# Kernel tuning notes

Hardware: AMD Instinct MI355X
Metric: run time of the kernel (lower is better)

## Reference

```python
import jax, jax.numpy as jnp
import numpy as np

NUM_HEADS = 8
MODEL_DIM = 1024
SEQ_LEN = 2048


def setup_inputs() -> dict:
    key = jax.random.key(0)
    ks = jax.random.split(key, 9)
    H, D, L = NUM_HEADS, MODEL_DIM, SEQ_LEN
    s_in = 1.0 / np.sqrt(D)
    s_out = 1.0 / np.sqrt(H * D)
    return {
        "tokens": jax.random.normal(ks[0], (D, L), dtype=jnp.float32),
        "Wq": jax.random.uniform(ks[1], (H * D, D), jnp.float32, -s_in, s_in),
        "bq": jax.random.uniform(ks[2], (H * D,), jnp.float32, -s_in, s_in),
        "Wk": jax.random.uniform(ks[3], (H * D, D), jnp.float32, -s_in, s_in),
        "bk": jax.random.uniform(ks[4], (H * D,), jnp.float32, -s_in, s_in),
        "Wv": jax.random.uniform(ks[5], (H * D, D), jnp.float32, -s_in, s_in),
        "bv": jax.random.uniform(ks[6], (H * D,), jnp.float32, -s_in, s_in),
        "Wo": jax.random.uniform(ks[7], (D, H * D), jnp.float32, -s_out, s_out),
        "bo": jax.random.uniform(ks[8], (D,), jnp.float32, -s_out, s_out),
    }


def _split_heads(x, H, D, L):
    # Faithful to torch: raw .view of contiguous [H*D, L] into (L, H, D),
    # then permute(1, 2, 0) -> (H, D, L). This is a memory reinterpretation,
    # not a transpose, exactly as in the original module.
    return x.reshape(L, H, D).transpose(1, 2, 0)


def reference(tokens, Wq, bq, Wk, bk, Wv, bv, Wo, bo):
    D, L = tokens.shape
    H = Wq.shape[0] // D
    # 1x1 Conv1d == matmul over channel dim
    q = _split_heads(Wq @ tokens + bq[:, None], H, D, L)  # (H, D, L)
    k = _split_heads(Wk @ tokens + bk[:, None], H, D, L)  # (H, D, L)
    v = _split_heads(Wv @ tokens + bv[:, None], H, D, L)  # (H, D, L)
    scores = jnp.einsum("hdl,hdm->hlm", q, k) / np.sqrt(D)  # (H, L, L)
    # torch F.softmax without dim on a 3D tensor -> dim=0 (head axis)
    attn = jax.nn.softmax(scores, axis=0)
    ctx = jnp.einsum("hlm,hdm->hdl", attn, v)  # (H, D, L)
    out = Wo @ ctx.reshape(H * D, L) + bo[:, None]  # (D, L)
    return out
```

## Files before the change

### kernel.cpp

```cpp
#include <hip/hip_runtime.h>

#define SEQL 2048
#define DMODEL 1024
#define HDIM 8192

typedef unsigned short bf16_t;
typedef __attribute__((ext_vector_type(8))) short bf16x8;
typedef __attribute__((ext_vector_type(4))) float f32x4;

__device__ __forceinline__ bf16_t f2bf(float f) {
  unsigned u = __float_as_uint(f);
  u += 0x7fffu + ((u >> 16) & 1u);
  return (bf16_t)(u >> 16);
}
__device__ __forceinline__ float bf2f(bf16_t b) {
  return __uint_as_float(((unsigned)b) << 16);
}

__global__ __launch_bounds__(256) void cvt_f32_bf16(const float* __restrict__ in,
                                                    bf16_t* __restrict__ out, int n) {
  int i = (blockIdx.x * 256 + threadIdx.x) * 4;
  if (i >= n) return;
  float4 f = *reinterpret_cast<const float4*>(in + i);
  ushort4 u;
  u.x = f2bf(f.x); u.y = f2bf(f.y); u.z = f2bf(f.z); u.w = f2bf(f.w);
  *reinterpret_cast<ushort4*>(out + i) = u;
}

__global__ __launch_bounds__(256) void cvt3_f32_bf16(const float* __restrict__ a,
                                                     const float* __restrict__ b,
                                                     const float* __restrict__ c,
                                                     bf16_t* __restrict__ out) {
  const int SEG = HDIM * DMODEL;
  int i = (blockIdx.x * 256 + threadIdx.x) * 4;
  const float* src;
  int off;
  if (i < SEG) { src = a; off = i; }
  else if (i < 2 * SEG) { src = b; off = i - SEG; }
  else { src = c; off = i - 2 * SEG; }
  float4 f = *reinterpret_cast<const float4*>(src + off);
  ushort4 u;
  u.x = f2bf(f.x); u.y = f2bf(f.y); u.z = f2bf(f.z); u.w = f2bf(f.w);
  *reinterpret_cast<ushort4*>(out + i) = u;
}

__global__ __launch_bounds__(256) void bias3(const float* __restrict__ a,
                                             const float* __restrict__ b,
                                             const float* __restrict__ c,
                                             float* __restrict__ out) {
  int i = blockIdx.x * 256 + threadIdx.x;
  float v = (i < HDIM) ? a[i] : (i < 2 * HDIM) ? b[i - HDIM] : c[i - 2 * HDIM];
  out[i] = v;
}

__global__ __launch_bounds__(256) void transpose_cvt(const float* __restrict__ in,
                                                     bf16_t* __restrict__ out) {
  __shared__ float tile[32][33];
  int bx = blockIdx.x * 32;
  int by = blockIdx.y * 32;
  int tx = threadIdx.x, ty = threadIdx.y;
#pragma unroll
  for (int i = ty; i < 32; i += 8)
    tile[i][tx] = in[(size_t)(by + i) * SEQL + bx + tx];
  __syncthreads();
#pragma unroll
  for (int i = ty; i < 32; i += 8)
    out[(size_t)(bx + i) * DMODEL + by + tx] = f2bf(tile[tx][i]);
}

__global__ __launch_bounds__(256) void softmax_heads(bf16_t* __restrict__ S) {
  const size_t HS = (size_t)SEQL * SEQL;
  size_t p = ((size_t)blockIdx.x * 256 + threadIdx.x) * 8;
  float v[8][8];
#pragma unroll
  for (int h = 0; h < 8; ++h) {
    bf16x8 x = *reinterpret_cast<const bf16x8*>(S + h * HS + p);
#pragma unroll
    for (int e = 0; e < 8; ++e) v[h][e] = bf2f((bf16_t)x[e]);
  }
#pragma unroll
  for (int e = 0; e < 8; ++e) {
    float mx = v[0][e];
#pragma unroll
    for (int h = 1; h < 8; ++h) mx = fmaxf(mx, v[h][e]);
    float s = 0.f;
#pragma unroll
    for (int h = 0; h < 8; ++h) { v[h][e] = __expf(v[h][e] - mx); s += v[h][e]; }
    float inv = 1.0f / s;
#pragma unroll
    for (int h = 0; h < 8; ++h) v[h][e] *= inv;
  }
#pragma unroll
  for (int h = 0; h < 8; ++h) {
    bf16x8 x;
#pragma unroll
    for (int e = 0; e < 8; ++e) x[e] = (short)f2bf(v[h][e]);
    *reinterpret_cast<bf16x8*>(S + h * HS + p) = x;
  }
}

__global__ __launch_bounds__(256) void reduce_out(const float* __restrict__ P,
                                                  const float* __restrict__ bo,
                                                  float* __restrict__ out) {
  const size_t NEL = (size_t)DMODEL * SEQL;
  size_t i = ((size_t)blockIdx.x * 256 + threadIdx.x) * 4;
  float4 a = *reinterpret_cast<const float4*>(P + i);
#pragma unroll
  for (int z = 1; z < 8; ++z) {
    float4 b = *reinterpret_cast<const float4*>(P + z * NEL + i);
    a.x += b.x; a.y += b.y; a.z += b.z; a.w += b.w;
  }
  float bias = bo[i / SEQL];
  a.x += bias; a.y += bias; a.z += bias; a.w += bias;
  *reinterpret_cast<float4*>(out + i) = a;
}

template <typename OutT, int EPI, bool HAS_BIAS>
__global__ __launch_bounds__(512, 2) void gemm256(
    const bf16_t* __restrict__ A, const bf16_t* __restrict__ B,
    OutT* __restrict__ C, bf16_t* __restrict__ C2, const float* __restrict__ bias,
    int K, int lda, int ldb, int ldc,
    long long sA, long long sB, long long sC, float scale, int gx, int gxy) {
  __shared__ alignas(16) char smem[147456];
  auto* As = reinterpret_cast<bf16_t(*)[2][8192]>(smem);
  auto* Bs = reinterpret_cast<bf16_t(*)[2][8192]>(smem + 65536);
  const int nwg = gridDim.x;
  const int bid = blockIdx.x;
  const int swz = (nwg & 7) ? bid : ((bid & 7) * (nwg >> 3) + (bid >> 3));
  const int zz = swz / gxy;
  const int rem = swz - zz * gxy;
  const int brow = (rem / gx) * 256;
  const int bcol = (rem % gx) * 256;
  A += (long long)zz * sA;
  B += (long long)zz * sB;
  C += (long long)zz * sC;
  const int tid = threadIdx.x;
  const int w = tid >> 6, lane = tid & 63;
  const int fr = lane & 15, fq = lane >> 4;
  const int wr = w >> 2, wc = w & 3;

  int rj[2], cj[2];
#pragma unroll
  for (int j = 0; j < 2; ++j) {
    const int c = (w * 2 + j) * 64 + lane;
    rj[j] = c >> 3;
    cj[j] = ((c & 7) ^ (rj[j] & 7)) << 3;
  }

  auto stageA = [&](int buf, int half, int kk) {
#pragma unroll
    for (int j = 0; j < 2; ++j) {
      const bf16_t* g = A + (size_t)(brow + half * 128 + rj[j]) * lda + kk + cj[j];
      __builtin_amdgcn_global_load_lds(
          (const __attribute__((address_space(1))) void*)g,
          (__attribute__((address_space(3))) void*)(&As[buf][half][(w * 2 + j) * 512]),
          16, 0, 0);
    }
  };
  auto stageB = [&](int buf, int half, int kk) {
#pragma unroll
    for (int j = 0; j < 2; ++j) {
      const bf16_t* g = B + (size_t)(bcol + half * 128 + rj[j]) * ldb + kk + cj[j];
      __builtin_amdgcn_global_load_lds(
          (const __attribute__((address_space(1))) void*)g,
          (__attribute__((address_space(3))) void*)(&Bs[buf][half][(w * 2 + j) * 512]),
          16, 0, 0);
    }
  };

  auto ldA = [&](int buf, int mf, int kk) -> bf16x8 {
    const int rr = mf * 16 + fr;
    return *reinterpret_cast<const bf16x8*>(
        &As[buf][wr][rr * 64 + ((((kk << 2) | fq) ^ (rr & 7)) << 3)]);
  };
  auto ldB = [&](int buf, int nf, int kk) -> bf16x8 {
    const int rr = (wc & 1) * 64 + nf * 16 + fr;
    return *reinterpret_cast<const bf16x8*>(
        &Bs[buf][wc >> 1][rr * 64 + ((((kk << 2) | fq) ^ (rr & 7)) << 3)]);
  };

  f32x4 acc[8][4];
  const f32x4 fzero = {0.f, 0.f, 0.f, 0.f};
#pragma unroll
  for (int m = 0; m < 8; ++m)
#pragma unroll
    for (int n = 0; n < 4; ++n) acc[m][n] = fzero;

  const int NT = K >> 6;
  stageA(0, 0, 0); stageA(0, 1, 0); stageB(0, 0, 0); stageB(0, 1, 0);
  __syncthreads();

  for (int t = 0; t < NT; ++t) {
    const int p = t & 1, q = p ^ 1;
    const int kn = (t + 1) << 6;
    const bool pre = (t + 1 < NT);
    bf16x8 af[4][2], bg[4][2];

    if (pre) { stageA(q, 0, kn); stageA(q, 1, kn); }
#pragma unroll
    for (int mf = 0; mf < 4; ++mf)
#pragma unroll
      for (int kk = 0; kk < 2; ++kk) af[mf][kk] = ldA(p, mf, kk);
#pragma unroll
    for (int nf = 0; nf < 2; ++nf)
#pragma unroll
      for (int kk = 0; kk < 2; ++kk) bg[nf][kk] = ldB(p, nf, kk);
    __builtin_amdgcn_s_setprio(1);
#pragma unroll
    for (int mf = 0; mf < 4; ++mf)
#pragma unroll
      for (int nf = 0; nf < 2; ++nf)
#pragma unroll
        for (int kk = 0; kk < 2; ++kk)
          acc[mf][nf] = __builtin_amdgcn_mfma_f32_16x16x32_bf16(
              af[mf][kk], bg[nf][kk], acc[mf][nf], 0, 0, 0);
    __builtin_amdgcn_s_setprio(0);

    if (pre) { stageB(q, 0, kn); stageB(q, 1, kn); }
#pragma unroll
    for (int nf = 2; nf < 4; ++nf)
#pragma unroll
      for (int kk = 0; kk < 2; ++kk) bg[nf][kk] = ldB(p, nf, kk);
    __builtin_amdgcn_s_setprio(1);
#pragma unroll
    for (int mf = 0; mf < 4; ++mf)
#pragma unroll
      for (int nf = 2; nf < 4; ++nf)
#pragma unroll
        for (int kk = 0; kk < 2; ++kk)
          acc[mf][nf] = __builtin_amdgcn_mfma_f32_16x16x32_bf16(
              af[mf][kk], bg[nf][kk], acc[mf][nf], 0, 0, 0);
    __builtin_amdgcn_s_setprio(0);

#pragma unroll
    for (int mf = 0; mf < 4; ++mf)
#pragma unroll
      for (int kk = 0; kk < 2; ++kk) af[mf][kk] = ldA(p, mf + 4, kk);
    __builtin_amdgcn_s_setprio(1);
#pragma unroll
    for (int mf = 0; mf < 4; ++mf)
#pragma unroll
      for (int nf = 2; nf < 4; ++nf)
#pragma unroll
        for (int kk = 0; kk < 2; ++kk)
          acc[mf + 4][nf] = __builtin_amdgcn_mfma_f32_16x16x32_bf16(
              af[mf][kk], bg[nf][kk], acc[mf + 4][nf], 0, 0, 0);
    __builtin_amdgcn_s_setprio(0);

#pragma unroll
    for (int nf = 0; nf < 2; ++nf)
#pragma unroll
      for (int kk = 0; kk < 2; ++kk) bg[nf][kk] = ldB(p, nf, kk);
    __builtin_amdgcn_s_setprio(1);
#pragma unroll
    for (int mf = 0; mf < 4; ++mf)
#pragma unroll
      for (int nf = 0; nf < 2; ++nf)
#pragma unroll
        for (int kk = 0; kk < 2; ++kk)
          acc[mf + 4][nf] = __builtin_amdgcn_mfma_f32_16x16x32_bf16(
              af[mf][kk], bg[nf][kk], acc[mf + 4][nf], 0, 0, 0);
    __builtin_amdgcn_s_setprio(0);

    if (pre) __syncthreads();
  }

  __syncthreads();

  const bool vseg = (EPI == 2) && (brow >= 2 * HDIM);
  if ((EPI == 0) || ((EPI == 2) && !vseg)) {
    bf16_t* Ct = (bf16_t*)smem;
#pragma unroll
    for (int mf = 0; mf < 8; ++mf)
#pragma unroll
      for (int j = 0; j < 4; ++j) {
        const int orow = wr * 128 + mf * 16 + fq * 4 + j;
        float bvv = HAS_BIAS ? bias[brow + orow] : 0.f;
#pragma unroll
        for (int nf = 0; nf < 4; ++nf)
          Ct[orow * 264 + wc * 64 + nf * 16 + fr] = f2bf(acc[mf][nf][j] * scale + bvv);
      }
    __syncthreads();
    bf16_t* Cb = (bf16_t*)C;
#pragma unroll
    for (int i = 0; i < 16; ++i) {
      const int c = tid + i * 512;
      const int row = c >> 5, ch = c & 31;
      *reinterpret_cast<bf16x8*>(&Cb[(size_t)(brow + row) * ldc + bcol + ch * 8]) =
          *reinterpret_cast<const bf16x8*>(smem + row * 528 + ch * 16);
    }
  } else if constexpr (EPI == 1) {
    float* Cf = (float*)smem;
#pragma unroll
    for (int h = 0; h < 2; ++h) {
      if (wr == h) {
#pragma unroll
        for (int mf = 0; mf < 8; ++mf)
#pragma unroll
          for (int j = 0; j < 4; ++j) {
            const int orow = mf * 16 + fq * 4 + j;
            float bvv = HAS_BIAS ? bias[brow + h * 128 + orow] : 0.f;
#pragma unroll
            for (int nf = 0; nf < 4; ++nf)
              Cf[orow * 264 + wc * 64 + nf * 16 + fr] = acc[mf][nf][j] * scale + bvv;
          }
      }
      __syncthreads();
#pragma unroll
      for (int i = 0; i < 16; ++i) {
        const int c = tid + i * 512;
        const int row = c >> 6, ch = c & 63;
        *reinterpret_cast<float4*>(&C[(size_t)(brow + h * 128 + row) * ldc + bcol + ch * 4]) =
            *reinterpret_cast<const float4*>(smem + row * 1056 + ch * 16);
      }
      __syncthreads();
    }
  } else if constexpr (EPI == 2) {
    const int vrow = brow - 2 * HDIM;
    bf16_t* Vt = (bf16_t*)smem;
#pragma unroll
    for (int mf = 0; mf < 8; ++mf)
#pragma unroll
      for (int j = 0; j < 4; ++j) {
        const int i = wr * 128 + mf * 16 + fq * 4 + j;
        const int mloc = i >> 2;
        float bvv = HAS_BIAS ? bias[brow + i] : 0.f;
#pragma unroll
        for (int nf = 0; nf < 4; ++nf) {
          const int dloc = wc * 64 + nf * 16 + fr;
          Vt[(j * 256 + dloc) * 72 + mloc] = f2bf(acc[mf][nf][j] * scale + bvv);
        }
      }
    __syncthreads();
    const int r_ = bcol >> 10, d0 = bcol & 1023, m0 = vrow >> 2;
#pragma unroll
    for (int sIt = 0; sIt < 2; ++sIt) {
      const int s = tid + sIt * 512;
      const int h2 = s >> 8, dloc = s & 255;
      const bf16_t* src = Vt + (h2 * 256 + dloc) * 72;
      bf16_t* dst = C2 + ((size_t)(2 * h2 + r_) * DMODEL + d0 + dloc) * SEQL + m0;
#pragma unroll
      for (int qq = 0; qq < 8; ++qq)
        *reinterpret_cast<bf16x8*>(dst + qq * 8) =
            *reinterpret_cast<const bf16x8*>(src + qq * 8);
    }
  }
}

extern "C" void kernel_launch(void* const* d_in, const int* in_sizes, int n_in,
                              void* d_out, int out_size, void* d_ws, size_t ws_size,
                              hipStream_t stream) {
  const float* tokens = (const float*)d_in[0];
  const float* Wq = (const float*)d_in[1];
  const float* bq = (const float*)d_in[2];
  const float* Wk = (const float*)d_in[3];
  const float* bk = (const float*)d_in[4];
  const float* Wv = (const float*)d_in[5];
  const float* bv = (const float*)d_in[6];
  const float* Wo = (const float*)d_in[7];
  const float* bo = (const float*)d_in[8];
  float* out = (float*)d_out;
  char* ws = (char*)d_ws;
  const size_t MB = 1024ull * 1024ull;
  bf16_t* Vs = (bf16_t*)(ws + 0);
  bf16_t* QmKm = (bf16_t*)(ws + 32 * MB);
  bf16_t* Qm = QmKm;
  bf16_t* Km = QmKm + (size_t)HDIM * SEQL;
  bf16_t* Sb = (bf16_t*)(ws + 96 * MB);
  bf16_t* tT = (bf16_t*)(ws + 96 * MB);
  bf16_t* Wqkv = (bf16_t*)(ws + 100 * MB);
  float* bqkv = (float*)(ws + 148 * MB);
  bf16_t* cT = (bf16_t*)(ws + 32 * MB);
  bf16_t* Wob = (bf16_t*)(ws + 64 * MB);
  float* Pp = (float*)(ws + 96 * MB);

  dim3 b256(256);
  dim3 b512(512);
  const int nW = HDIM * DMODEL;

  transpose_cvt<<<dim3(SEQL / 32, DMODEL / 32), dim3(32, 8), 0, stream>>>(tokens, tT);
  cvt3_f32_bf16<<<3 * nW / 1024, b256, 0, stream>>>(Wq, Wk, Wv, Wqkv);
  bias3<<<3 * HDIM / 256, b256, 0, stream>>>(bq, bk, bv, bqkv);

  gemm256<bf16_t, 2, true><<<dim3(768, 1, 1), b512, 0, stream>>>(
      Wqkv, tT, QmKm, Vs, bqkv, DMODEL, DMODEL, DMODEL, SEQL,
      0, 0, 0, 1.0f, 8, 768);

  gemm256<bf16_t, 0, false><<<dim3(512, 1, 1), b512, 0, stream>>>(
      Qm, Km, Sb, nullptr, nullptr, DMODEL, HDIM, HDIM, SEQL,
      1024, 1024, (long long)SEQL * SEQL, 0.03125f, 8, 64);

  softmax_heads<<<(SEQL * SEQL / 8) / 256, b256, 0, stream>>>(Sb);

  gemm256<bf16_t, 0, false><<<dim3(256, 1, 1), b512, 0, stream>>>(
      Sb, Vs, cT, nullptr, nullptr, SEQL, SEQL, SEQL, HDIM,
      (long long)SEQL * SEQL, (long long)DMODEL * SEQL, 1024, 1.0f, 4, 32);

  cvt_f32_bf16<<<nW / 1024, b256, 0, stream>>>(Wo, Wob, nW);
  gemm256<float, 1, false><<<dim3(256, 1, 1), b512, 0, stream>>>(
      Wob, cT, Pp, nullptr, nullptr, 1024, HDIM, HDIM, SEQL,
      1024, 1024, (long long)DMODEL * SEQL, 1.0f, 8, 32);
  reduce_out<<<(DMODEL * SEQL / 4) / 256, b256, 0, stream>>>(Pp, bo, out);
}
```

Baseline: 366.6 us.

## Fuse fp32 weight-to-bf16 conversion into GEMM A-tile loads, store bf16 partials

Removes the separate weight conversion kernels for Wq/Wk/Wv and Wo. The GEMM now loads fp32 A tiles into registers during the previous iteration, converts them to bf16 and writes them to LDS before the barrier. The split-K output partials for the Wo projection are stored as bf16 instead of fp32, which halves the traffic into reduce_out. The cost is register-staged A loads that no longer use direct-to-LDS copies, and reduced precision in the partial sums.

Result: slower. 382.3 us (+4.3%).

```diff
diff --git a/kernel.cpp b/kernel.cpp
--- a/kernel.cpp
+++ b/kernel.cpp
@@ -15,33 +15,6 @@
 }
 __device__ __forceinline__ float bf2f(bf16_t b) {
   return __uint_as_float(((unsigned)b) << 16);
-}
-
-__global__ __launch_bounds__(256) void cvt_f32_bf16(const float* __restrict__ in,
-                                                    bf16_t* __restrict__ out, int n) {
-  int i = (blockIdx.x * 256 + threadIdx.x) * 4;
-  if (i >= n) return;
-  float4 f = *reinterpret_cast<const float4*>(in + i);
-  ushort4 u;
-  u.x = f2bf(f.x); u.y = f2bf(f.y); u.z = f2bf(f.z); u.w = f2bf(f.w);
-  *reinterpret_cast<ushort4*>(out + i) = u;
-}
-
-__global__ __launch_bounds__(256) void cvt3_f32_bf16(const float* __restrict__ a,
-                                                     const float* __restrict__ b,
-                                                     const float* __restrict__ c,
-                                                     bf16_t* __restrict__ out) {
-  const int SEG = HDIM * DMODEL;
-  int i = (blockIdx.x * 256 + threadIdx.x) * 4;
-  const float* src;
-  int off;
-  if (i < SEG) { src = a; off = i; }
-  else if (i < 2 * SEG) { src = b; off = i - SEG; }
-  else { src = c; off = i - 2 * SEG; }
-  float4 f = *reinterpret_cast<const float4*>(src + off);
-  ushort4 u;
-  u.x = f2bf(f.x); u.y = f2bf(f.y); u.z = f2bf(f.z); u.w = f2bf(f.w);
-  *reinterpret_cast<ushort4*>(out + i) = u;
 }
 
 __global__ __launch_bounds__(256) void bias3(const float* __restrict__ a,
@@ -99,26 +72,29 @@
   }
 }
 
-__global__ __launch_bounds__(256) void reduce_out(const float* __restrict__ P,
+__global__ __launch_bounds__(256) void reduce_out(const bf16_t* __restrict__ P,
                                                   const float* __restrict__ bo,
                                                   float* __restrict__ out) {
   const size_t NEL = (size_t)DMODEL * SEQL;
-  size_t i = ((size_t)blockIdx.x * 256 + threadIdx.x) * 4;
-  float4 a = *reinterpret_cast<const float4*>(P + i);
-#pragma unroll
-  for (int z = 1; z < 8; ++z) {
-    float4 b = *reinterpret_cast<const float4*>(P + z * NEL + i);
-    a.x += b.x; a.y += b.y; a.z += b.z; a.w += b.w;
-  }
-  float bias = bo[i / SEQL];
-  a.x += bias; a.y += bias; a.z += bias; a.w += bias;
-  *reinterpret_cast<float4*>(out + i) = a;
-}
-
-template <typename OutT, int EPI, bool HAS_BIAS>
+  size_t i = ((size_t)blockIdx.x * 256 + threadIdx.x) * 8;
+  float s[8] = {0.f, 0.f, 0.f, 0.f, 0.f, 0.f, 0.f, 0.f};
+#pragma unroll
+  for (int z = 0; z < 8; ++z) {
+    bf16x8 x = *reinterpret_cast<const bf16x8*>(P + z * NEL + i);
+#pragma unroll
+    for (int e = 0; e < 8; ++e) s[e] += bf2f((bf16_t)x[e]);
+  }
+  float bias = bo[i >> 11];
+  float4 o0 = {s[0] + bias, s[1] + bias, s[2] + bias, s[3] + bias};
+  float4 o1 = {s[4] + bias, s[5] + bias, s[6] + bias, s[7] + bias};
+  *reinterpret_cast<float4*>(out + i) = o0;
+  *reinterpret_cast<float4*>(out + i + 4) = o1;
+}
+
+template <bool AF32, int EPI, bool HAS_BIAS>
 __global__ __launch_bounds__(512, 2) void gemm256(
-    const bf16_t* __restrict__ A, const bf16_t* __restrict__ B,
-    OutT* __restrict__ C, bf16_t* __restrict__ C2, const float* __restrict__ bias,
+    const void* Aq_, const void* Ak_, const void* Av_, const bf16_t* __restrict__ B,
+    bf16_t* __restrict__ C, bf16_t* __restrict__ C2, const float* __restrict__ bias,
     int K, int lda, int ldb, int ldc,
     long long sA, long long sB, long long sC, float scale, int gx, int gxy) {
   __shared__ alignas(16) char smem[147456];
@@ -131,7 +107,17 @@
   const int rem = swz - zz * gxy;
   const int brow = (rem / gx) * 256;
   const int bcol = (rem % gx) * 256;
-  A += (long long)zz * sA;
+  const bf16_t* Ab = nullptr;
+  const float* Af = nullptr;
+  int arow = brow;
+  if constexpr (AF32) {
+    const int seg = brow >> 13;
+    Af = (const float*)(seg == 0 ? Aq_ : (seg == 1 ? Ak_ : Av_));
+    Af += (long long)zz * sA;
+    arow = brow & 8191;
+  } else {
+    Ab = (const bf16_t*)Aq_ + (long long)zz * sA;
+  }
   B += (long long)zz * sB;
   C += (long long)zz * sC;
   const int tid = threadIdx.x;
@@ -150,12 +136,36 @@
   auto stageA = [&](int buf, int half, int kk) {
 #pragma unroll
     for (int j = 0; j < 2; ++j) {
-      const bf16_t* g = A + (size_t)(brow + half * 128 + rj[j]) * lda + kk + cj[j];
+      const bf16_t* g = Ab + (size_t)(brow + half * 128 + rj[j]) * lda + kk + cj[j];
       __builtin_amdgcn_global_load_lds(
           (const __attribute__((address_space(1))) void*)g,
           (__attribute__((address_space(3))) void*)(&As[buf][half][(w * 2 + j) * 512]),
           16, 0, 0);
     }
+  };
+  float4 fa[2][2][2];
+  auto ALOAD = [&](int kk) {
+#pragma unroll
+    for (int half = 0; half < 2; ++half)
+#pragma unroll
+      for (int j = 0; j < 2; ++j) {
+        const float* g = Af + (size_t)(arow + half * 128 + rj[j]) * lda + kk + cj[j];
+        fa[half][j][0] = *reinterpret_cast<const float4*>(g);
+        fa[half][j][1] = *reinterpret_cast<const float4*>(g + 4);
+      }
+  };
+  auto AWRITE = [&](int buf) {
+#pragma unroll
+    for (int half = 0; half < 2; ++half)
+#pragma unroll
+      for (int j = 0; j < 2; ++j) {
+        bf16x8 v;
+        v[0] = (short)f2bf(fa[half][j][0].x); v[1] = (short)f2bf(fa[half][j][0].y);
+        v[2] = (short)f2bf(fa[half][j][0].z); v[3] = (short)f2bf(fa[half][j][0].w);
+        v[4] = (short)f2bf(fa[half][j][1].x); v[5] = (short)f2bf(fa[half][j][1].y);
+        v[6] = (short)f2bf(fa[half][j][1].z); v[7] = (short)f2bf(fa[half][j][1].w);
+        *reinterpret_cast<bf16x8*>(&As[buf][half][(w * 2 + j) * 512 + lane * 8]) = v;
+      }
   };
   auto stageB = [&](int buf, int half, int kk) {
 #pragma unroll
@@ -187,7 +197,9 @@
     for (int n = 0; n < 4; ++n) acc[m][n] = fzero;
 
   const int NT = K >> 6;
-  stageA(0, 0, 0); stageA(0, 1, 0); stageB(0, 0, 0); stageB(0, 1, 0);
+  if constexpr (AF32) { ALOAD(0); AWRITE(0); }
+  else { stageA(0, 0, 0); stageA(0, 1, 0); }
+  stageB(0, 0, 0); stageB(0, 1, 0);
   __syncthreads();
 
   for (int t = 0; t < NT; ++t) {
@@ -196,7 +208,10 @@
     const bool pre = (t + 1 < NT);
     bf16x8 af[4][2], bg[4][2];
 
-    if (pre) { stageA(q, 0, kn); stageA(q, 1, kn); }
+    if (pre) {
+      if constexpr (AF32) ALOAD(kn);
+      else { stageA(q, 0, kn); stageA(q, 1, kn); }
+    }
 #pragma unroll
     for (int mf = 0; mf < 4; ++mf)
 #pragma unroll
@@ -262,7 +277,10 @@
               af[mf][kk], bg[nf][kk], acc[mf + 4][nf], 0, 0, 0);
     __builtin_amdgcn_s_setprio(0);
 
-    if (pre) __syncthreads();
+    if (pre) {
+      if constexpr (AF32) AWRITE(q);
+      __syncthreads();
+    }
   }
 
   __syncthreads();
@@ -281,39 +299,12 @@
           Ct[orow * 264 + wc * 64 + nf * 16 + fr] = f2bf(acc[mf][nf][j] * scale + bvv);
       }
     __syncthreads();
-    bf16_t* Cb = (bf16_t*)C;
 #pragma unroll
     for (int i = 0; i < 16; ++i) {
       const int c = tid + i * 512;
       const int row = c >> 5, ch = c & 31;
-      *reinterpret_cast<bf16x8*>(&Cb[(size_t)(brow + row) * ldc + bcol + ch * 8]) =
+      *reinterpret_cast<bf16x8*>(&C[(size_t)(brow + row) * ldc + bcol + ch * 8]) =
           *reinterpret_cast<const bf16x8*>(smem + row * 528 + ch * 16);
-    }
-  } else if constexpr (EPI == 1) {
-    float* Cf = (float*)smem;
-#pragma unroll
-    for (int h = 0; h < 2; ++h) {
-      if (wr == h) {
-#pragma unroll
-        for (int mf = 0; mf < 8; ++mf)
-#pragma unroll
-          for (int j = 0; j < 4; ++j) {
-            const int orow = mf * 16 + fq * 4 + j;
-            float bvv = HAS_BIAS ? bias[brow + h * 128 + orow] : 0.f;
-#pragma unroll
-            for (int nf = 0; nf < 4; ++nf)
-              Cf[orow * 264 + wc * 64 + nf * 16 + fr] = acc[mf][nf][j] * scale + bvv;
-          }
-      }
-      __syncthreads();
-#pragma unroll
-      for (int i = 0; i < 16; ++i) {
-        const int c = tid + i * 512;
-        const int row = c >> 6, ch = c & 63;
-        *reinterpret_cast<float4*>(&C[(size_t)(brow + h * 128 + row) * ldc + bcol + ch * 4]) =
-            *reinterpret_cast<const float4*>(smem + row * 1056 + ch * 16);
-      }
-      __syncthreads();
     }
   } else if constexpr (EPI == 2) {
     const int vrow = brow - 2 * HDIM;
@@ -368,37 +359,32 @@
   bf16_t* Km = QmKm + (size_t)HDIM * SEQL;
   bf16_t* Sb = (bf16_t*)(ws + 96 * MB);
   bf16_t* tT = (bf16_t*)(ws + 96 * MB);
-  bf16_t* Wqkv = (bf16_t*)(ws + 100 * MB);
-  float* bqkv = (float*)(ws + 148 * MB);
+  float* bqkv = (float*)(ws + 100 * MB);
   bf16_t* cT = (bf16_t*)(ws + 32 * MB);
-  bf16_t* Wob = (bf16_t*)(ws + 64 * MB);
-  float* Pp = (float*)(ws + 96 * MB);
+  bf16_t* Pp = (bf16_t*)(ws + 96 * MB);
 
   dim3 b256(256);
   dim3 b512(512);
-  const int nW = HDIM * DMODEL;
 
   transpose_cvt<<<dim3(SEQL / 32, DMODEL / 32), dim3(32, 8), 0, stream>>>(tokens, tT);
-  cvt3_f32_bf16<<<3 * nW / 1024, b256, 0, stream>>>(Wq, Wk, Wv, Wqkv);
   bias3<<<3 * HDIM / 256, b256, 0, stream>>>(bq, bk, bv, bqkv);
 
-  gemm256<bf16_t, 2, true><<<dim3(768, 1, 1), b512, 0, stream>>>(
-      Wqkv, tT, QmKm, Vs, bqkv, DMODEL, DMODEL, DMODEL, SEQL,
+  gemm256<true, 2, true><<<dim3(768, 1, 1), b512, 0, stream>>>(
+      Wq, Wk, Wv, tT, QmKm, Vs, bqkv, DMODEL, DMODEL, DMODEL, SEQL,
       0, 0, 0, 1.0f, 8, 768);
 
-  gemm256<bf16_t, 0, false><<<dim3(512, 1, 1), b512, 0, stream>>>(
-      Qm, Km, Sb, nullptr, nullptr, DMODEL, HDIM, HDIM, SEQL,
+  gemm256<false, 0, false><<<dim3(512, 1, 1), b512, 0, stream>>>(
+      Qm, nullptr, nullptr, Km, Sb, nullptr, nullptr, DMODEL, HDIM, HDIM, SEQL,
       1024, 1024, (long long)SEQL * SEQL, 0.03125f, 8, 64);
 
   softmax_heads<<<(SEQL * SEQL / 8) / 256, b256, 0, stream>>>(Sb);
 
-  gemm256<bf16_t, 0, false><<<dim3(256, 1, 1), b512, 0, stream>>>(
-      Sb, Vs, cT, nullptr, nullptr, SEQL, SEQL, SEQL, HDIM,
+  gemm256<false, 0, false><<<dim3(256, 1, 1), b512, 0, stream>>>(
+      Sb, nullptr, nullptr, Vs, cT, nullptr, nullptr, SEQL, SEQL, SEQL, HDIM,
       (long long)SEQL * SEQL, (long long)DMODEL * SEQL, 1024, 1.0f, 4, 32);
 
-  cvt_f32_bf16<<<nW / 1024, b256, 0, stream>>>(Wo, Wob, nW);
-  gemm256<float, 1, false><<<dim3(256, 1, 1), b512, 0, stream>>>(
-      Wob, cT, Pp, nullptr, nullptr, 1024, HDIM, HDIM, SEQL,
+  gemm256<true, 0, false><<<dim3(256, 1, 1), b512, 0, stream>>>(
+      Wo, nullptr, nullptr, cT, Pp, nullptr, nullptr, 1024, HDIM, HDIM, SEQL,
       1024, 1024, (long long)DMODEL * SEQL, 1.0f, 8, 32);
-  reduce_out<<<(DMODEL * SEQL / 4) / 256, b256, 0, stream>>>(Pp, bo, out);
-}
+  reduce_out<<<(DMODEL * SEQL / 8) / 256, b256, 0, stream>>>(Pp, bo, out);
+}
```
